# Kernel optimization log

Measured on AMD Instinct MI355X. Metric: run time of the kernel, lower is better.

## Reference

```python
import jax, jax.numpy as jnp
import numpy as np

N_NODES = 50000
N_EDGES = 600000
N_SUB = 20000
E_SUB = 120000
D = 128

def setup_inputs() -> dict:
    key = jax.random.key(0)
    ks = jax.random.split(key, 16)
    s = 1.0 / np.sqrt(D)
    inp = {
        "x": jax.random.normal(ks[0], (N_NODES, D), dtype=jnp.float32),
        "Wm": jax.random.normal(ks[1], (D, D), dtype=jnp.float32) * s,
        "bm": jnp.zeros((D,), dtype=jnp.float32),
        "Wn2s0": jax.random.normal(ks[2], (D, D), dtype=jnp.float32) * s,
        "bn2s0": jnp.zeros((D,), dtype=jnp.float32),
        "Ws2n0": jax.random.normal(ks[3], (D, D), dtype=jnp.float32) * s,
        "bs2n0": jnp.zeros((D,), dtype=jnp.float32),
        "Wn2s1": jax.random.normal(ks[4], (D, D), dtype=jnp.float32) * s,
        "bn2s1": jnp.zeros((D,), dtype=jnp.float32),
        "Ws2n1": jax.random.normal(ks[5], (D, D), dtype=jnp.float32) * s,
        "bs2n1": jnp.zeros((D,), dtype=jnp.float32),
        "neighbor_edge_index": jax.random.randint(ks[6], (2, N_EDGES), 0, N_NODES, dtype=jnp.int64),
        "sub_row0": jax.random.randint(ks[7], (E_SUB,), 0, N_NODES, dtype=jnp.int64),
        "sub_col0": jax.random.randint(ks[8], (E_SUB,), 0, N_SUB, dtype=jnp.int64),
        "sub_row1": jax.random.randint(ks[9], (E_SUB,), 0, N_NODES, dtype=jnp.int64),
        "sub_col1": jax.random.randint(ks[10], (E_SUB,), 0, N_SUB, dtype=jnp.int64),
    }
    return inp


def _level(x, row, col, Wn2s, bn2s, Ws2n, bs2n):
    # node -> substructure: gather node feats, sum-reduce into substructures
    sub_x = jax.ops.segment_sum(x[row], col, num_segments=N_SUB)  # [n_sub, D]
    sub_x = sub_x @ Wn2s + bn2s
    # substructure -> node: gather substructure feats, sum-reduce back to nodes
    msg = jax.ops.segment_sum(sub_x[col], row, num_segments=N_NODES)  # [N, D]
    msg = msg @ Ws2n + bs2n
    return x + msg


def reference(x, Wm, bm, Wn2s0, bn2s0, Ws2n0, bs2n0, Wn2s1, bn2s1, Ws2n1, bs2n1,
              neighbor_edge_index, sub_row0, sub_col0, sub_row1, sub_col1):
    src, dst = neighbor_edge_index[0], neighbor_edge_index[1]
    # message_neighbor: GIN-like sum aggregation + Linear + ReLU
    agg = jax.ops.segment_sum(x[src], dst, num_segments=N_NODES)
    x = jax.nn.relu((x + agg) @ Wm + bm)
    # substructure levels (gather -> scatter-sum -> Linear -> gather -> scatter-sum -> Linear -> residual)
    x = _level(x, sub_row0, sub_col0, Wn2s0, bn2s0, Ws2n0, bs2n0)
    x = _level(x, sub_row1, sub_col1, Wn2s1, bn2s1, Ws2n1, bs2n1)
    return x
```

## Files before the change

### kernel.cpp

```cpp
#include <hip/hip_runtime.h>

#define D 128
#define NN 50000
#define NS 20000
#define NNP 50048
#define NSP 20032
#define L_TOT (3 * NN + 2 * NS)
#define SCAN_CHUNK 1024
#define SCAN_NBLK ((L_TOT + SCAN_CHUNK - 1) / SCAN_CHUNK)
#define LDA 136

typedef short s16x8 __attribute__((ext_vector_type(8)));
typedef float f32x4 __attribute__((ext_vector_type(4)));

__device__ __forceinline__ float b2f(unsigned int u) {
    u <<= 16;
    float f; __builtin_memcpy(&f, &u, 4);
    return f;
}
__device__ __forceinline__ unsigned short f2b(float f) {
    unsigned int u; __builtin_memcpy(&u, &f, 4);
    u += 0x7fffu + ((u >> 16) & 1u);
    return (unsigned short)(u >> 16);
}
__device__ __forceinline__ void acc8(float* a, uint4 v) {
    a[0] += b2f(v.x & 0xffffu); a[1] += b2f(v.x >> 16);
    a[2] += b2f(v.y & 0xffffu); a[3] += b2f(v.y >> 16);
    a[4] += b2f(v.z & 0xffffu); a[5] += b2f(v.z >> 16);
    a[6] += b2f(v.w & 0xffffu); a[7] += b2f(v.w >> 16);
}

#define NX4 (NN * D / 4)
#define NW  (5 * 16384)
#define PREP_N (NX4 + NW)
#define PREP_BLOCKS ((PREP_N + 255) / 256)

struct PrepHistArgs {
    const float* x; unsigned short* xb;
    const float* w[5]; unsigned short* wt[5];
    const int* s0; const int* s1; const int* s2; const int* s3; const int* s4;
    int* counts; unsigned short* rank;
    int nE, eS;
};
__global__ __launch_bounds__(256) void preph_k(PrepHistArgs p)
{
    int bid = blockIdx.x;
    if (bid < PREP_BLOCKS) {
        int i = bid * 256 + threadIdx.x;
        if (i < NX4) {
            float4 v = ((const float4*)p.x)[i];
            ushort4 o;
            o.x = f2b(v.x); o.y = f2b(v.y); o.z = f2b(v.z); o.w = f2b(v.w);
            ((ushort4*)p.xb)[i] = o;
            return;
        }
        i -= NX4;
        if (i < NW) {
            int wi = i >> 14;
            int r  = i & 16383;
            int k = r >> 7, n = r & 127;
            p.wt[wi][n * 128 + k] = f2b(p.w[wi][k * 128 + n]);
        }
        return;
    }
    int e = (bid - PREP_BLOCKS) * 256 + threadIdx.x;
    int seg, base;
    if (e < p.nE) { seg = p.s0[e]; base = 0; }
    else {
        int r = e - p.nE;
        if      (r <     p.eS) { seg = p.s1[r];            base = NN; }
        else if (r < 2 * p.eS) { seg = p.s2[r - p.eS];     base = NN + NS; }
        else if (r < 3 * p.eS) { seg = p.s3[r - 2 * p.eS]; base = 2 * NN + NS; }
        else if (r < 4 * p.eS) { seg = p.s4[r - 3 * p.eS]; base = 2 * NN + 2 * NS; }
        else return;
    }
    p.rank[e] = (unsigned short)atomicAdd(&p.counts[base + seg], 1);
}

__global__ __launch_bounds__(256) void reduce_k(const int* __restrict__ counts,
                                                int* __restrict__ blockSums, int n)
{
    __shared__ int lds[4];
    int tid = threadIdx.x;
    int base = blockIdx.x * SCAN_CHUNK;
    int s = 0;
    #pragma unroll
    for (int i = 0; i < 4; ++i) {
        int idx = base + tid + i * 256;
        if (idx < n) s += counts[idx];
    }
    #pragma unroll
    for (int off = 32; off > 0; off >>= 1) s += __shfl_down(s, off, 64);
    if ((tid & 63) == 0) lds[tid >> 6] = s;
    __syncthreads();
    if (tid == 0) blockSums[blockIdx.x] = lds[0] + lds[1] + lds[2] + lds[3];
}

__global__ __launch_bounds__(256) void scan_sums_k(int* __restrict__ blockSums, int nb)
{
    __shared__ int lds[256];
    int tid = threadIdx.x;
    lds[tid] = (tid < nb) ? blockSums[tid] : 0;
    __syncthreads();
    for (int off = 1; off < 256; off <<= 1) {
        int t = (tid >= off) ? lds[tid - off] : 0;
        __syncthreads();
        lds[tid] += t;
        __syncthreads();
    }
    if (tid < nb) blockSums[tid] = (tid > 0) ? lds[tid - 1] : 0;
}

__global__ __launch_bounds__(256) void scan_write_k(
    const int* __restrict__ counts, const int* __restrict__ blockSums,
    int* __restrict__ offsets, int n)
{
    __shared__ int lds[256];
    int tid = threadIdx.x;
    int base = blockIdx.x * SCAN_CHUNK + tid * 4;
    int v[4]; int s = 0;
    #pragma unroll
    for (int i = 0; i < 4; ++i) {
        int idx = base + i;
        int c = (idx < n) ? counts[idx] : 0;
        v[i] = c; s += c;
    }
    lds[tid] = s;
    __syncthreads();
    for (int off = 1; off < 256; off <<= 1) {
        int t = (tid >= off) ? lds[tid - off] : 0;
        __syncthreads();
        lds[tid] += t;
        __syncthreads();
    }
    int run = blockSums[blockIdx.x] + (tid > 0 ? lds[tid - 1] : 0);
    #pragma unroll
    for (int i = 0; i < 4; ++i) {
        int idx = base + i;
        run += v[i];
        if (idx < n) offsets[idx + 1] = run;
    }
    if (blockIdx.x == 0 && tid == 0) offsets[0] = 0;
}

__global__ __launch_bounds__(256) void fill5_k(
    const int* __restrict__ s0, const int* __restrict__ v0,
    const int* __restrict__ s1, const int* __restrict__ v1,
    const int* __restrict__ s2, const int* __restrict__ v2,
    const int* __restrict__ s3, const int* __restrict__ v3,
    const int* __restrict__ s4, const int* __restrict__ v4,
    const int* __restrict__ offsets, const unsigned short* __restrict__ rank,
    unsigned short* __restrict__ perm, int nE, int eS)
{
    int e = blockIdx.x * 256 + threadIdx.x;
    int seg, val, base;
    if (e < nE) { seg = s0[e]; val = v0[e]; base = 0; }
    else {
        int r = e - nE;
        if      (r <     eS) { seg = s1[r];          val = v1[r];          base = NN; }
        else if (r < 2 * eS) { seg = s2[r - eS];     val = v2[r - eS];     base = NN + NS; }
        else if (r < 3 * eS) { seg = s3[r - 2 * eS]; val = v3[r - 2 * eS]; base = 2 * NN + NS; }
        else if (r < 4 * eS) { seg = s4[r - 3 * eS]; val = v4[r - 3 * eS]; base = 2 * NN + 2 * NS; }
        else return;
    }
    perm[offsets[base + seg] + (int)rank[e]] = (unsigned short)val;
}

__global__ __launch_bounds__(256, 7) void gg_k(
    const unsigned short* __restrict__ feat, const int* __restrict__ offsets,
    const unsigned short* __restrict__ perm, const unsigned short* __restrict__ addend,
    const unsigned short* __restrict__ Wt, const float* __restrict__ bias,
    const unsigned short* __restrict__ Rb,
    float* __restrict__ outF, unsigned short* __restrict__ outB,
    int M, int relu)
{
    __shared__ unsigned short a_lds[64 * LDA];

    const int tid = threadIdx.x;
    const int r0  = blockIdx.x * 64;

    const uint4* f4 = (const uint4*)feat;
    const int lane16 = tid & 15;
    #pragma unroll
    for (int p = 0; p < 4; ++p) {
        int rloc = p * 16 + (tid >> 4);
        int s = r0 + rloc;
        float a[8] = {0.f, 0.f, 0.f, 0.f, 0.f, 0.f, 0.f, 0.f};
        if (s < M) {
            float b[8] = {0.f, 0.f, 0.f, 0.f, 0.f, 0.f, 0.f, 0.f};
            if (addend) {
                uint4 v = ((const uint4*)(addend + (size_t)s * D))[lane16];
                acc8(a, v);
            }
            int beg = offsets[s], end = offsets[s + 1];
            int j = beg;
            for (; j + 3 < end; j += 4) {
                int e0 = perm[j], e1 = perm[j + 1], e2 = perm[j + 2], e3 = perm[j + 3];
                uint4 v0 = f4[(size_t)e0 * 16 + lane16];
                uint4 v1 = f4[(size_t)e1 * 16 + lane16];
                uint4 v2 = f4[(size_t)e2 * 16 + lane16];
                uint4 v3 = f4[(size_t)e3 * 16 + lane16];
                acc8(a, v0); acc8(b, v1); acc8(a, v2); acc8(b, v3);
            }
            for (; j < end; ++j)
                acc8(a, f4[(size_t)perm[j] * 16 + lane16]);
            #pragma unroll
            for (int i = 0; i < 8; ++i) a[i] += b[i];
        }
        uint4 o;
        o.x = (unsigned int)f2b(a[0]) | ((unsigned int)f2b(a[1]) << 16);
        o.y = (unsigned int)f2b(a[2]) | ((unsigned int)f2b(a[3]) << 16);
        o.z = (unsigned int)f2b(a[4]) | ((unsigned int)f2b(a[5]) << 16);
        o.w = (unsigned int)f2b(a[6]) | ((unsigned int)f2b(a[7]) << 16);
        *((uint4*)&a_lds[rloc * LDA + lane16 * 8]) = o;
    }
    __syncthreads();

    const int lane = tid & 63;
    const int w    = tid >> 6;
    const int ln   = lane & 15;
    const int quad = lane >> 4;

    s16x8 af[4];
    const unsigned short* arow = &a_lds[(w * 16 + ln) * LDA + quad * 8];
    #pragma unroll
    for (int kc = 0; kc < 4; ++kc)
        af[kc] = *((const s16x8*)(arow + kc * 32));

    const int rbase = r0 + w * 16 + quad * 4;
    const s16x8* wt8 = (const s16x8*)Wt;

    #pragma unroll
    for (int nt = 0; nt < 8; ++nt) {
        f32x4 acc = {0.f, 0.f, 0.f, 0.f};
        const s16x8* brow = wt8 + (nt * 16 + ln) * 16 + quad;
        #pragma unroll
        for (int kc = 0; kc < 4; ++kc) {
            s16x8 bf = brow[kc * 4];
            acc = __builtin_amdgcn_mfma_f32_16x16x32_bf16(af[kc], bf, acc, 0, 0, 0);
        }
        int col = nt * 16 + ln;
        float bc = bias[col];
        #pragma unroll
        for (int r = 0; r < 4; ++r) {
            int row = rbase + r;
            if (row < M) {
                float v = acc[r] + bc;
                size_t gi = (size_t)row * D + col;
                if (Rb) v += b2f((unsigned int)Rb[gi]);
                if (relu) v = fmaxf(v, 0.f);
                if (outF) outF[gi] = v;
                if (outB) outB[gi] = f2b(v);
            }
        }
    }
}

extern "C" void kernel_launch(void* const* d_in, const int* in_sizes, int n_in,
                              void* d_out, int out_size, void* d_ws, size_t ws_size,
                              hipStream_t stream)
{
    const float* x     = (const float*)d_in[0];
    const float* Wm    = (const float*)d_in[1];
    const float* bm    = (const float*)d_in[2];
    const float* Wn2s0 = (const float*)d_in[3];
    const float* bn2s0 = (const float*)d_in[4];
    const float* Ws2n0 = (const float*)d_in[5];
    const float* bs2n0 = (const float*)d_in[6];
    const float* Wn2s1 = (const float*)d_in[7];
    const float* bn2s1 = (const float*)d_in[8];
    const float* Ws2n1 = (const float*)d_in[9];
    const float* bs2n1 = (const float*)d_in[10];
    const int* nei  = (const int*)d_in[11];
    const int* row0 = (const int*)d_in[12];
    const int* col0 = (const int*)d_in[13];
    const int* row1 = (const int*)d_in[14];
    const int* col1 = (const int*)d_in[15];

    const int N_E = in_sizes[11] / 2;
    const int E_S = in_sizes[12];
    const int TOT_E = N_E + 4 * E_S;

    const int* src = nei;
    const int* dst = nei + N_E;

    float* out = (float*)d_out;

    unsigned short* xb   = (unsigned short*)d_ws;
    unsigned short* hbf  = xb  + (size_t)NNP * D;
    unsigned short* subb = hbf + (size_t)NNP * D;
    unsigned short* wtb  = subb + (size_t)NSP * D;
    unsigned short* rank = wtb + 5 * 16384;
    unsigned short* perm = rank + ((TOT_E + 1) & ~1);
    int* ip      = (int*)(perm + ((TOT_E + 1) & ~1));
    int* counts  = ip;              ip += L_TOT;
    int* offsets = ip;              ip += L_TOT + 1;
    int* bsums   = ip;              ip += 256;

    unsigned short* wt0 = wtb;
    unsigned short* wt1 = wtb + 16384;
    unsigned short* wt2 = wtb + 2 * 16384;
    unsigned short* wt3 = wtb + 3 * 16384;
    unsigned short* wt4 = wtb + 4 * 16384;

    const int* offB  = offsets;
    const int* off0c = offsets + NN;
    const int* off0r = offsets + NN + NS;
    const int* off1c = offsets + 2 * NN + NS;
    const int* off1r = offsets + 2 * NN + 2 * NS;

    dim3 blk(256);
    dim3 gTot((TOT_E + 255) / 256);
    dim3 gGemmN(NNP / 64);
    dim3 gGemmS(NSP / 64);
    dim3 gPrepH(PREP_BLOCKS + (TOT_E + 255) / 256);

    hipMemsetAsync(counts, 0, L_TOT * sizeof(int), stream);
    PrepHistArgs pa;
    pa.x = x; pa.xb = xb;
    pa.w[0] = Wm;  pa.w[1] = Wn2s0; pa.w[2] = Ws2n0; pa.w[3] = Wn2s1; pa.w[4] = Ws2n1;
    pa.wt[0] = wt0; pa.wt[1] = wt1; pa.wt[2] = wt2; pa.wt[3] = wt3; pa.wt[4] = wt4;
    pa.s0 = dst; pa.s1 = col0; pa.s2 = row0; pa.s3 = col1; pa.s4 = row1;
    pa.counts = counts; pa.rank = rank;
    pa.nE = N_E; pa.eS = E_S;
    preph_k<<<gPrepH, blk, 0, stream>>>(pa);

    reduce_k<<<SCAN_NBLK, blk, 0, stream>>>(counts, bsums, L_TOT);
    scan_sums_k<<<1, blk, 0, stream>>>(bsums, SCAN_NBLK);
    scan_write_k<<<SCAN_NBLK, blk, 0, stream>>>(counts, bsums, offsets, L_TOT);
    fill5_k<<<gTot, blk, 0, stream>>>(dst, src, col0, row0, row0, col0,
                                      col1, row1, row1, col1, offsets, rank,
                                      perm, N_E, E_S);

    gg_k<<<gGemmN, blk, 0, stream>>>(xb, offB, perm, xb, wt0, bm,
                                     nullptr, nullptr, hbf, NN, 1);

    gg_k<<<gGemmS, blk, 0, stream>>>(hbf, off0c, perm, nullptr, wt1, bn2s0,
                                     nullptr, nullptr, subb, NS, 0);
    gg_k<<<gGemmN, blk, 0, stream>>>(subb, off0r, perm, nullptr, wt2, bs2n0,
                                     hbf, nullptr, xb, NN, 0);

    gg_k<<<gGemmS, blk, 0, stream>>>(xb, off1c, perm, nullptr, wt3, bn2s1,
                                     nullptr, nullptr, subb, NS, 0);
    gg_k<<<gGemmN, blk, 0, stream>>>(subb, off1r, perm, nullptr, wt4, bs2n1,
                                     xb, out, nullptr, NN, 0);
}
```

Before: 342.3 us.

## Replicate histogram counters across eight slots to spread atomic contention

The per-segment edge counters are split into eight replicas, chosen by block index, so atomicAdds from different blocks hitting the same segment land on different addresses. The prefix scan now runs over the eight-times-larger interleaved counter array, using a 8192-element chunk staged through padded LDS. Fill and the gather-GEMM kernels index offsets at stride eight so each segment still maps to one contiguous range. This adds a larger memset, a larger scan, and strided offset reads, in exchange for what is probably only modest atomic contention at these graph sizes.

```diff
diff --git a/kernel.cpp b/kernel.cpp
--- a/kernel.cpp
+++ b/kernel.cpp
@@ -6,8 +6,10 @@
 #define NNP 50048
 #define NSP 20032
 #define L_TOT (3 * NN + 2 * NS)
-#define SCAN_CHUNK 1024
-#define SCAN_NBLK ((L_TOT + SCAN_CHUNK - 1) / SCAN_CHUNK)
+#define K_REP 8
+#define SCAN_N (L_TOT * K_REP)
+#define SCAN_CHUNK 8192
+#define SCAN_NBLK ((SCAN_N + SCAN_CHUNK - 1) / SCAN_CHUNK)
 #define LDA 136
 
 typedef short s16x8 __attribute__((ext_vector_type(8)));
@@ -74,7 +76,8 @@
         else if (r < 4 * p.eS) { seg = p.s4[r - 3 * p.eS]; base = 2 * NN + 2 * NS; }
         else return;
     }
-    p.rank[e] = (unsigned short)atomicAdd(&p.counts[base + seg], 1);
+    int k = (e >> 8) & (K_REP - 1);
+    p.rank[e] = (unsigned short)atomicAdd(&p.counts[((base + seg) << 3) | k], 1);
 }
 
 __global__ __launch_bounds__(256) void reduce_k(const int* __restrict__ counts,
@@ -85,8 +88,8 @@
     int base = blockIdx.x * SCAN_CHUNK;
     int s = 0;
     #pragma unroll
-    for (int i = 0; i < 4; ++i) {
-        int idx = base + tid + i * 256;
+    for (int i = 0; i < 32; ++i) {
+        int idx = base + i * 256 + tid;
         if (idx < n) s += counts[idx];
     }
     #pragma unroll
@@ -111,18 +114,26 @@
     if (tid < nb) blockSums[tid] = (tid > 0) ? lds[tid - 1] : 0;
 }
 
+#define SW_PAD(j) ((j) + ((j) >> 5))
+
 __global__ __launch_bounds__(256) void scan_write_k(
     const int* __restrict__ counts, const int* __restrict__ blockSums,
     int* __restrict__ offsets, int n)
 {
+    __shared__ int buf[SCAN_CHUNK + SCAN_CHUNK / 32];
     __shared__ int lds[256];
     int tid = threadIdx.x;
-    int base = blockIdx.x * SCAN_CHUNK + tid * 4;
-    int v[4]; int s = 0;
-    #pragma unroll
-    for (int i = 0; i < 4; ++i) {
-        int idx = base + i;
-        int c = (idx < n) ? counts[idx] : 0;
+    int cbase = blockIdx.x * SCAN_CHUNK;
+    #pragma unroll
+    for (int i = 0; i < 32; ++i) {
+        int idx = cbase + i * 256 + tid;
+        buf[SW_PAD(i * 256 + tid)] = (idx < n) ? counts[idx] : 0;
+    }
+    __syncthreads();
+    int v[32]; int s = 0;
+    #pragma unroll
+    for (int i = 0; i < 32; ++i) {
+        int c = buf[SW_PAD(tid * 32 + i)];
         v[i] = c; s += c;
     }
     lds[tid] = s;
@@ -135,10 +146,15 @@
     }
     int run = blockSums[blockIdx.x] + (tid > 0 ? lds[tid - 1] : 0);
     #pragma unroll
-    for (int i = 0; i < 4; ++i) {
-        int idx = base + i;
+    for (int i = 0; i < 32; ++i) {
         run += v[i];
-        if (idx < n) offsets[idx + 1] = run;
+        buf[SW_PAD(tid * 32 + i)] = run;
+    }
+    __syncthreads();
+    #pragma unroll
+    for (int i = 0; i < 32; ++i) {
+        int idx = cbase + i * 256 + tid;
+        if (idx < n) offsets[idx + 1] = buf[SW_PAD(i * 256 + tid)];
     }
     if (blockIdx.x == 0 && tid == 0) offsets[0] = 0;
 }
@@ -163,7 +179,8 @@
         else if (r < 4 * eS) { seg = s4[r - 3 * eS]; val = v4[r - 3 * eS]; base = 2 * NN + 2 * NS; }
         else return;
     }
-    perm[offsets[base + seg] + (int)rank[e]] = (unsigned short)val;
+    int k = (e >> 8) & (K_REP - 1);
+    perm[offsets[((base + seg) << 3) | k] + (int)rank[e]] = (unsigned short)val;
 }
 
 __global__ __launch_bounds__(256, 7) void gg_k(
@@ -192,7 +209,7 @@
                 uint4 v = ((const uint4*)(addend + (size_t)s * D))[lane16];
                 acc8(a, v);
             }
-            int beg = offsets[s], end = offsets[s + 1];
+            int beg = offsets[s << 3], end = offsets[(s + 1) << 3];
             int j = beg;
             for (; j + 3 < end; j += 4) {
                 int e0 = perm[j], e1 = perm[j + 1], e2 = perm[j + 2], e3 = perm[j + 3];
@@ -293,8 +310,8 @@
     unsigned short* rank = wtb + 5 * 16384;
     unsigned short* perm = rank + ((TOT_E + 1) & ~1);
     int* ip      = (int*)(perm + ((TOT_E + 1) & ~1));
-    int* counts  = ip;              ip += L_TOT;
-    int* offsets = ip;              ip += L_TOT + 1;
+    int* counts  = ip;              ip += L_TOT * K_REP;
+    int* offsets = ip;              ip += L_TOT * K_REP + 1;
     int* bsums   = ip;              ip += 256;
 
     unsigned short* wt0 = wtb;
@@ -304,10 +321,10 @@
     unsigned short* wt4 = wtb + 4 * 16384;
 
     const int* offB  = offsets;
-    const int* off0c = offsets + NN;
-    const int* off0r = offsets + NN + NS;
-    const int* off1c = offsets + 2 * NN + NS;
-    const int* off1r = offsets + 2 * NN + 2 * NS;
+    const int* off0c = offsets + (size_t)NN * K_REP;
+    const int* off0r = offsets + (size_t)(NN + NS) * K_REP;
+    const int* off1c = offsets + (size_t)(2 * NN + NS) * K_REP;
+    const int* off1r = offsets + (size_t)(2 * NN + 2 * NS) * K_REP;
 
     dim3 blk(256);
     dim3 gTot((TOT_E + 255) / 256);
@@ -315,7 +332,7 @@
     dim3 gGemmS(NSP / 64);
     dim3 gPrepH(PREP_BLOCKS + (TOT_E + 255) / 256);
 
-    hipMemsetAsync(counts, 0, L_TOT * sizeof(int), stream);
+    hipMemsetAsync(counts, 0, (size_t)L_TOT * K_REP * sizeof(int), stream);
     PrepHistArgs pa;
     pa.x = x; pa.xb = xb;
     pa.w[0] = Wm;  pa.w[1] = Wn2s0; pa.w[2] = Ws2n0; pa.w[3] = Wn2s1; pa.w[4] = Ws2n1;
@@ -325,9 +342,9 @@
     pa.nE = N_E; pa.eS = E_S;
     preph_k<<<gPrepH, blk, 0, stream>>>(pa);
 
-    reduce_k<<<SCAN_NBLK, blk, 0, stream>>>(counts, bsums, L_TOT);
+    reduce_k<<<SCAN_NBLK, blk, 0, stream>>>(counts, bsums, SCAN_N);
     scan_sums_k<<<1, blk, 0, stream>>>(bsums, SCAN_NBLK);
-    scan_write_k<<<SCAN_NBLK, blk, 0, stream>>>(counts, bsums, offsets, L_TOT);
+    scan_write_k<<<SCAN_NBLK, blk, 0, stream>>>(counts, bsums, offsets, SCAN_N);
     fill5_k<<<gTot, blk, 0, stream>>>(dst, src, col0, row0, row0, col0,
                                       col1, row1, row1, col1, offsets, rank,
                                       perm, N_E, E_S);
```

After: 360.0 us. 5.2% more time.
